# Optimization experiments

Hardware: AMD Instinct MI355X
Metric: run time of the kernel (lower is better)

The kernel has to match this reference:

```python
import jax, jax.numpy as jnp
import numpy as np

N = 8192      # nodes
E = 16384     # edges
G = 512       # graphs
IN = 235      # node feature dim (input_dim)
H = 64        # hidden_dim
ED = 52       # edge feature dim


def setup_inputs() -> dict:
    key = jax.random.key(0)
    ks = jax.random.split(key, 24)
    s = lambda fan_in: 1.0 / np.sqrt(fan_in)
    inp = {}
    inp["x"] = jax.random.normal(ks[0], (N, IN), dtype=jnp.float32)
    inp["edge_index"] = jax.random.randint(ks[1], (2, E), 0, N)
    inp["edge_attr"] = jax.random.uniform(ks[2], (E, ED), dtype=jnp.float32)
    inp["batch"] = jnp.sort(jax.random.randint(ks[3], (N,), 0, G))
    # EdgeModel (nn of nnconv1): Linear(52,128) -> Linear(128, 235*64)
    inp["W1"] = jax.random.normal(ks[4], (128, ED), dtype=jnp.float32) * s(ED)
    inp["b1"] = jnp.zeros((128,), jnp.float32)
    inp["W2"] = jax.random.normal(ks[5], (IN * H, 128), dtype=jnp.float32) * s(128)
    inp["b2"] = jnp.zeros((IN * H,), jnp.float32)
    # NNConv root weight and bias
    inp["root"] = jax.random.normal(ks[6], (IN, H), dtype=jnp.float32) * s(IN)
    inp["conv_b"] = jnp.zeros((H,), jnp.float32)
    # MLP head
    inp["fw1"] = jax.random.normal(ks[7], (128, H), dtype=jnp.float32) * s(H)
    inp["fb1"] = jnp.zeros((128,), jnp.float32)
    inp["fw2"] = jax.random.normal(ks[8], (256, 128), dtype=jnp.float32) * s(128)
    inp["fb2"] = jnp.zeros((256,), jnp.float32)
    inp["fw3"] = jax.random.normal(ks[9], (128, 256), dtype=jnp.float32) * s(256)
    inp["fb3"] = jnp.zeros((128,), jnp.float32)
    inp["fw4"] = jax.random.normal(ks[10], (1, 128), dtype=jnp.float32) * s(128)
    inp["fb4"] = jnp.zeros((1,), jnp.float32)
    return inp


def reference(x, edge_index, edge_attr, batch, W1, b1, W2, b2, root, conv_b,
              fw1, fb1, fw2, fb2, fw3, fb3, fw4, fb4):
    src, dst = edge_index[0], edge_index[1]
    # edge MLP -> per-edge weight matrices [E, IN, H]
    h = edge_attr @ W1.T + b1
    w = (h @ W2.T + b2).reshape(E, IN, H)
    # gather source node feats, per-edge matmul, scatter-add to destinations
    msg = jnp.einsum('ei,eih->eh', x[src], w)          # [E, H]
    agg = jax.ops.segment_sum(msg, dst, num_segments=N)  # [N, H]
    out = jax.nn.relu(agg + x @ root + conv_b)           # NNConv + ReLU
    # global mean pool per graph
    summ = jax.ops.segment_sum(out, batch, num_segments=G)
    cnt = jax.ops.segment_sum(jnp.ones((N, 1), out.dtype), batch, num_segments=G)
    pooled = summ / jnp.maximum(cnt, 1.0)                # [G, H]
    # dense MLP head
    y = jax.nn.relu(pooled @ fw1.T + fb1)
    y = jax.nn.relu(y @ fw2.T + fb2)
    y = jax.nn.relu(y @ fw3.T + fb3)
    return y @ fw4.T + fb4                               # [G, 1]
```

## Files before the change

kernel.cpp:

```cpp
#include <hip/hip_runtime.h>
#include <hip/hip_bf16.h>
#include <stdint.h>

#define N_NODES 8192
#define N_EDGES 16384
#define N_GRAPHS 512
#define IN_DIM 235
#define H_DIM 64
#define ED_DIM 52
#define HID1 128
#define KP 256
#define NB 3328
#define NBP 3584

#define BT_BLOCKS 940
#define EXT_BLOCKS 128
#define ZERO_BLOCKS 16
#define PREP_GRID (BT_BLOCKS + EXT_BLOCKS + ZERO_BLOCKS + N_NODES)

typedef __bf16 bf16x8 __attribute__((ext_vector_type(8)));
typedef float f32x4 __attribute__((ext_vector_type(4)));

static __device__ inline unsigned short f2bf(float f) {
    union { float f; unsigned u; } v; v.f = f;
    unsigned r = v.u + 0x7FFFu + ((v.u >> 16) & 1u);
    return (unsigned short)(r >> 16);
}

__global__ __launch_bounds__(256) void k_prep(const float* __restrict__ x,
                                              const float* __restrict__ W1,
                                              const float* __restrict__ W2,
                                              const float* __restrict__ b1,
                                              const float* __restrict__ b2,
                                              const float* __restrict__ root,
                                              unsigned short* __restrict__ A,
                                              unsigned short* __restrict__ Bt) {
    __shared__ float w1s[ED_DIM * 132];
    __shared__ float w2s[16 * 132];
    const int bx = blockIdx.x;
    const int t = threadIdx.x;

    if (bx < BT_BLOCKS) {
        const int i = bx >> 2;
        const int by = bx & 3;
        for (int j = t; j < ED_DIM * HID1; j += 256) {
            const int k = j / ED_DIM, d = j - k * ED_DIM;
            w1s[d * 132 + k] = W1[j];
        }
        const float* w2src = W2 + ((size_t)i * 64 + by * 16) * HID1;
        for (int j = t; j < 16 * HID1; j += 256) w2s[(j >> 7) * 132 + (j & 127)] = w2src[j];
        __syncthreads();
        const int hh = t & 15, dq = t >> 4;
        const float4* w2v = (const float4*)&w2s[hh * 132];
        #pragma unroll
        for (int m = 0; m < 4; ++m) {
            const int d = dq + m * 16;
            if (d >= ED_DIM) break;
            const float4* w1v = (const float4*)&w1s[d * 132];
            float acc = 0.f;
            #pragma unroll
            for (int k4 = 0; k4 < HID1 / 4; ++k4) {
                const float4 a = w1v[k4], b = w2v[k4];
                acc += a.x * b.x + a.y * b.y + a.z * b.z + a.w * b.w;
            }
            const int p = (by * 16 + hh) * ED_DIM + d;
            Bt[(size_t)p * KP + i] = f2bf(acc);
        }
    } else if (bx < BT_BLOCKS + EXT_BLOCKS) {
        const int j = bx - BT_BLOCKS;
        const int i = t;
        if (i < IN_DIM) {
            float v;
            if (j < 64) {
                v = root[i * H_DIM + j];
            } else {
                const int jj = i * H_DIM + (j - 64);
                float acc = b2[jj];
                const float* w = W2 + (size_t)jj * HID1;
                #pragma unroll 8
                for (int k = 0; k < HID1; ++k) acc += w[k] * b1[k];
                v = acc;
            }
            Bt[(size_t)(NB + j) * KP + i] = f2bf(v);
        }
    } else if (bx < BT_BLOCKS + EXT_BLOCKS + ZERO_BLOCKS) {
        const int z = bx - BT_BLOCKS - EXT_BLOCKS;
        const int R1 = NBP * 21;
        const int TOT = R1 + 128 * IN_DIM;
        for (int idx = z * 256 + t; idx < TOT; idx += ZERO_BLOCKS * 256) {
            size_t off;
            if (idx < R1) {
                const int r = idx / 21, c = IN_DIM + idx - (idx / 21) * 21;
                off = (size_t)r * KP + c;
            } else {
                const int k = idx - R1;
                const int r = 3456 + k / IN_DIM, c = k - (k / IN_DIM) * IN_DIM;
                off = (size_t)r * KP + c;
            }
            Bt[off] = 0;
        }
    } else {
        const int j = (bx - BT_BLOCKS - EXT_BLOCKS - ZERO_BLOCKS) * 256 + t;
        const int n = j >> 8, i = j & 255;
        A[j] = (i < IN_DIM) ? f2bf(x[n * IN_DIM + i]) : (unsigned short)0;
    }
}

__global__ __launch_bounds__(1024, 4) void k_gemm(const unsigned short* __restrict__ A,
                                                  const unsigned short* __restrict__ Bt,
                                                  unsigned short* __restrict__ P,
                                                  float* __restrict__ agg,
                                                  float* __restrict__ xb2,
                                                  const float* __restrict__ conv_b) {
    __shared__ unsigned short As[2 * 256 * 32];
    __shared__ unsigned short Bs[2 * 256 * 32];
    const int t = threadIdx.x;
    const int lin = blockIdx.x;
    const int xcd = lin & 7, bi = lin >> 3;
    const int mt = (bi / 14) * 8 + xcd;
    const int nt = bi % 14;
    const int m0 = mt * 256, n0 = nt * 256;
    const int wid = t >> 6, lane = t & 63;
    const int wm = wid & 3;
    const int wn = wid >> 2;
    const int q = lane >> 4, r16 = lane & 15;

    f32x4 acc[4][4] = {};

    auto stage = [&](int k0, int buf) {
        const int idx = t;
        const int row = idx >> 2;
        const int lgrp = ((idx & 3) ^ ((row >> 1) & 3)) * 8;
        const unsigned short* ga = &A[(size_t)(m0 + row) * KP + k0 + lgrp];
        const unsigned short* gb = &Bt[(size_t)(n0 + row) * KP + k0 + lgrp];
        char* la = (char*)As + buf * 16384 + wid * 1024;
        char* lb = (char*)Bs + buf * 16384 + wid * 1024;
        __builtin_amdgcn_global_load_lds(
            (const __attribute__((address_space(1))) unsigned int*)ga,
            (__attribute__((address_space(3))) unsigned int*)la, 16, 0, 0);
        __builtin_amdgcn_global_load_lds(
            (const __attribute__((address_space(1))) unsigned int*)gb,
            (__attribute__((address_space(3))) unsigned int*)lb, 16, 0, 0);
    };

    stage(0, 0);
    const int pcq = (q ^ ((r16 >> 1) & 3)) * 8;
    #pragma unroll
    for (int it = 0; it < 8; ++it) {
        __syncthreads();
        if (it < 7) stage((it + 1) * 32, (it + 1) & 1);
        const int bo = (it & 1) * 8192;
        bf16x8 af[4], bfr[4];
        #pragma unroll
        for (int mi = 0; mi < 4; ++mi)
            af[mi] = *(const bf16x8*)(&As[bo + (wm * 64 + mi * 16 + r16) * 32 + pcq]);
        #pragma unroll
        for (int ni = 0; ni < 4; ++ni)
            bfr[ni] = *(const bf16x8*)(&Bs[bo + (wn * 64 + ni * 16 + r16) * 32 + pcq]);
        #pragma unroll
        for (int mi = 0; mi < 4; ++mi)
            #pragma unroll
            for (int ni = 0; ni < 4; ++ni)
                acc[mi][ni] = __builtin_amdgcn_mfma_f32_16x16x32_bf16(
                    bfr[ni], af[mi], acc[mi][ni], 0, 0, 0);
    }

    if (n0 < NB) {
        #pragma unroll
        for (int mi = 0; mi < 4; ++mi)
            #pragma unroll
            for (int ni = 0; ni < 4; ++ni) {
                const int row = m0 + wm * 64 + mi * 16 + r16;
                const int col = n0 + wn * 64 + ni * 16 + q * 4;
                union { unsigned short us[4]; uint2 u2; } pk;
                #pragma unroll
                for (int rr = 0; rr < 4; ++rr) pk.us[rr] = f2bf(acc[mi][ni][rr]);
                *(uint2*)(&P[(size_t)row * NB + col]) = pk.u2;
            }
    } else if (wn < 2) {
        #pragma unroll
        for (int mi = 0; mi < 4; ++mi)
            #pragma unroll
            for (int ni = 0; ni < 4; ++ni) {
                const int row = m0 + wm * 64 + mi * 16 + r16;
                const int cl = ni * 16 + q * 4;
                if (wn == 0) {
                    const float4 cb = *(const float4*)&conv_b[cl];
                    float4 v;
                    v.x = acc[mi][ni][0] + cb.x; v.y = acc[mi][ni][1] + cb.y;
                    v.z = acc[mi][ni][2] + cb.z; v.w = acc[mi][ni][3] + cb.w;
                    *(float4*)(&agg[row * H_DIM + cl]) = v;
                } else {
                    float4 v;
                    v.x = acc[mi][ni][0]; v.y = acc[mi][ni][1];
                    v.z = acc[mi][ni][2]; v.w = acc[mi][ni][3];
                    *(float4*)(&xb2[row * H_DIM + cl]) = v;
                }
            }
    }
}

__global__ __launch_bounds__(256) void k_edge(const int* __restrict__ ei,
                                              const float* __restrict__ ea,
                                              const unsigned short* __restrict__ P,
                                              const float* __restrict__ xb2,
                                              float* __restrict__ agg) {
    const int e = (blockIdx.x * 256 + threadIdx.x) >> 6;
    const int h = threadIdx.x & 63;
    if (e >= N_EDGES) return;
    const int s = ei[e], dst = ei[N_EDGES + e];
    const uint2* Pr = (const uint2*)(P + (size_t)s * NB + h * ED_DIM);
    const float4* ev = (const float4*)(ea + (size_t)e * ED_DIM);

    uint2 pv[13];
    #pragma unroll
    for (int j = 0; j < 13; ++j) pv[j] = Pr[j];
    float4 eav[13];
    #pragma unroll
    for (int j = 0; j < 13; ++j) eav[j] = ev[j];

    float acc = xb2[s * H_DIM + h];
    #pragma unroll
    for (int j = 0; j < 13; ++j) {
        union { unsigned u; float f; } a0, a1, b0, b1;
        a0.u = pv[j].x << 16; a1.u = pv[j].x & 0xffff0000u;
        b0.u = pv[j].y << 16; b1.u = pv[j].y & 0xffff0000u;
        acc += eav[j].x * a0.f + eav[j].y * a1.f
             + eav[j].z * b0.f + eav[j].w * b1.f;
    }
    atomicAdd(&agg[dst * H_DIM + h], acc);
}

__global__ __launch_bounds__(256) void k_tail(const float* __restrict__ agg,
                                              const int* __restrict__ batch,
                                              const float* __restrict__ fw1, const float* __restrict__ fb1,
                                              const float* __restrict__ fw2, const float* __restrict__ fb2,
                                              const float* __restrict__ fw3, const float* __restrict__ fb3,
                                              const float* __restrict__ fw4, const float* __restrict__ fb4,
                                              float* __restrict__ out) {
    __shared__ float red[256];
    __shared__ float sp[64], s1[128], s2[256], s3[128];
    const int g = blockIdx.x, t = threadIdx.x;

    int lo = 0, hi = N_NODES;
    while (lo < hi) { const int mid = (lo + hi) >> 1; if (batch[mid] < g) lo = mid + 1; else hi = mid; }
    const int start = lo;
    hi = N_NODES;
    while (lo < hi) { const int mid = (lo + hi) >> 1; if (batch[mid] <= g) lo = mid + 1; else hi = mid; }
    const int end = lo;
    const float inv = 1.0f / fmaxf((float)(end - start), 1.0f);

    float a = 0.f;
    for (int n = start + (t >> 6); n < end; n += 4)
        a += fmaxf(agg[n * H_DIM + (t & 63)], 0.f);
    red[t] = a;
    __syncthreads();
    if (t < 64) sp[t] = (red[t] + red[t + 64] + red[t + 128] + red[t + 192]) * inv;
    __syncthreads();

    if (t < 128) {
        float acc = fb1[t];
        const float* w = fw1 + t * 64;
        #pragma unroll 8
        for (int k = 0; k < 64; ++k) acc += sp[k] * w[k];
        s1[t] = fmaxf(acc, 0.f);
    }
    __syncthreads();
    {
        float acc = fb2[t];
        const float* w = fw2 + t * 128;
        #pragma unroll 8
        for (int k = 0; k < 128; ++k) acc += s1[k] * w[k];
        s2[t] = fmaxf(acc, 0.f);
    }
    __syncthreads();
    if (t < 128) {
        float acc = fb3[t];
        const float* w = fw3 + t * 256;
        #pragma unroll 8
        for (int k = 0; k < 256; ++k) acc += s2[k] * w[k];
        s3[t] = fmaxf(acc, 0.f);
    }
    __syncthreads();
    if (t < 64) {
        float p = s3[t] * fw4[t] + s3[t + 64] * fw4[t + 64];
        #pragma unroll
        for (int off = 32; off > 0; off >>= 1) p += __shfl_down(p, off);
        if (t == 0) out[g] = p + fb4[0];
    }
}

extern "C" void kernel_launch(void* const* d_in, const int* in_sizes, int n_in,
                              void* d_out, int out_size, void* d_ws, size_t ws_size,
                              hipStream_t stream) {
    const float* x      = (const float*)d_in[0];
    const int*   ei     = (const int*)d_in[1];
    const float* ea     = (const float*)d_in[2];
    const int*   batch  = (const int*)d_in[3];
    const float* W1     = (const float*)d_in[4];
    const float* b1     = (const float*)d_in[5];
    const float* W2     = (const float*)d_in[6];
    const float* b2     = (const float*)d_in[7];
    const float* root   = (const float*)d_in[8];
    const float* conv_b = (const float*)d_in[9];
    const float* fw1 = (const float*)d_in[10]; const float* fb1 = (const float*)d_in[11];
    const float* fw2 = (const float*)d_in[12]; const float* fb2 = (const float*)d_in[13];
    const float* fw3 = (const float*)d_in[14]; const float* fb3 = (const float*)d_in[15];
    const float* fw4 = (const float*)d_in[16]; const float* fb4 = (const float*)d_in[17];
    float* out = (float*)d_out;

    char* ws = (char*)d_ws;
    unsigned short* A   = (unsigned short*)(ws);
    unsigned short* Bt  = (unsigned short*)(ws + 4194304);
    unsigned short* P   = (unsigned short*)(ws + 6029312);
    float* agg  = (float*)(ws + 60555264);
    float* xb2  = (float*)(ws + 62652416);

    k_prep<<<dim3(PREP_GRID), dim3(256), 0, stream>>>(x, W1, W2, b1, b2, root, A, Bt);
    k_gemm<<<dim3(448), dim3(1024), 0, stream>>>(A, Bt, P, agg, xb2, conv_b);
    k_edge<<<dim3(N_EDGES / 4), dim3(256), 0, stream>>>(ei, ea, P, xb2, agg);
    k_tail<<<dim3(N_GRAPHS), dim3(256), 0, stream>>>(agg, batch, fw1, fb1, fw2, fb2, fw3, fb3, fw4, fb4, out);
}
```

Before: 185.5 us.

## Shrink GEMM tiles to 128x128, interleave P layout, vectorize prep and tail

The GEMM tile drops from 256x256 with 1024 threads to 128x128 with 256 threads, over a 1728-block grid. This gives more, smaller blocks and removes the 1/4 idle-tail waste on the extension columns. The Bt/P column layout is permuted so that each edge thread reads P with a stride of 64 uint2, coalescing the per-edge gathers, and the zero-padding logic is simplified to match. The prep kernel converts x to bf16 eight elements per thread, and the bias-fold and tail MLP loops use float4 loads. Smaller tiles lower data reuse per block and raise global traffic for A and Bt.

```diff
diff --git a/kernel.cpp b/kernel.cpp
--- a/kernel.cpp
+++ b/kernel.cpp
@@ -13,10 +13,14 @@
 #define NB 3328
 #define NBP 3584
 
+
 #define BT_BLOCKS 940
 #define EXT_BLOCKS 128
 #define ZERO_BLOCKS 16
-#define PREP_GRID (BT_BLOCKS + EXT_BLOCKS + ZERO_BLOCKS + N_NODES)
+#define A_BLOCKS 1024
+#define PREP_GRID (BT_BLOCKS + EXT_BLOCKS + ZERO_BLOCKS + A_BLOCKS)
+
+#define GEMM_GRID 1728
 
 typedef __bf16 bf16x8 __attribute__((ext_vector_type(8)));
 typedef float f32x4 __attribute__((ext_vector_type(4)));
@@ -51,6 +55,7 @@
         for (int j = t; j < 16 * HID1; j += 256) w2s[(j >> 7) * 132 + (j & 127)] = w2src[j];
         __syncthreads();
         const int hh = t & 15, dq = t >> 4;
+        const int h = by * 16 + hh;
         const float4* w2v = (const float4*)&w2s[hh * 132];
         #pragma unroll
         for (int m = 0; m < 4; ++m) {
@@ -63,7 +68,7 @@
                 const float4 a = w1v[k4], b = w2v[k4];
                 acc += a.x * b.x + a.y * b.y + a.z * b.z + a.w * b.w;
             }
-            const int p = (by * 16 + hh) * ED_DIM + d;
+            const int p = ((d >> 2) << 8) + h * 4 + (d & 3);
             Bt[(size_t)p * KP + i] = f2bf(acc);
         }
     } else if (bx < BT_BLOCKS + EXT_BLOCKS) {
@@ -76,71 +81,76 @@
             } else {
                 const int jj = i * H_DIM + (j - 64);
                 float acc = b2[jj];
-                const float* w = W2 + (size_t)jj * HID1;
-                #pragma unroll 8
-                for (int k = 0; k < HID1; ++k) acc += w[k] * b1[k];
+                const float4* w = (const float4*)(W2 + (size_t)jj * HID1);
+                const float4* bv = (const float4*)b1;
+                #pragma unroll
+                for (int k4 = 0; k4 < HID1 / 4; ++k4) {
+                    const float4 a = w[k4], b = bv[k4];
+                    acc += a.x * b.x; acc += a.y * b.y; acc += a.z * b.z; acc += a.w * b.w;
+                }
                 v = acc;
             }
             Bt[(size_t)(NB + j) * KP + i] = f2bf(v);
         }
     } else if (bx < BT_BLOCKS + EXT_BLOCKS + ZERO_BLOCKS) {
         const int z = bx - BT_BLOCKS - EXT_BLOCKS;
-        const int R1 = NBP * 21;
-        const int TOT = R1 + 128 * IN_DIM;
+        const int TOT = 3456 * 21;
         for (int idx = z * 256 + t; idx < TOT; idx += ZERO_BLOCKS * 256) {
-            size_t off;
-            if (idx < R1) {
-                const int r = idx / 21, c = IN_DIM + idx - (idx / 21) * 21;
-                off = (size_t)r * KP + c;
-            } else {
-                const int k = idx - R1;
-                const int r = 3456 + k / IN_DIM, c = k - (k / IN_DIM) * IN_DIM;
-                off = (size_t)r * KP + c;
-            }
-            Bt[off] = 0;
+            const int r = idx / 21, c = IN_DIM + idx - r * 21;
+            Bt[(size_t)r * KP + c] = 0;
         }
     } else {
-        const int j = (bx - BT_BLOCKS - EXT_BLOCKS - ZERO_BLOCKS) * 256 + t;
-        const int n = j >> 8, i = j & 255;
-        A[j] = (i < IN_DIM) ? f2bf(x[n * IN_DIM + i]) : (unsigned short)0;
-    }
-}
-
-__global__ __launch_bounds__(1024, 4) void k_gemm(const unsigned short* __restrict__ A,
-                                                  const unsigned short* __restrict__ Bt,
-                                                  unsigned short* __restrict__ P,
-                                                  float* __restrict__ agg,
-                                                  float* __restrict__ xb2,
-                                                  const float* __restrict__ conv_b) {
-    __shared__ unsigned short As[2 * 256 * 32];
-    __shared__ unsigned short Bs[2 * 256 * 32];
+        const int j8 = (bx - BT_BLOCKS - EXT_BLOCKS - ZERO_BLOCKS) * 256 + t;
+        const int n = j8 >> 5, i0 = (j8 & 31) * 8;
+        const float* xr = x + (size_t)n * IN_DIM;
+        union { unsigned short us[8]; uint4 q; } pk;
+        #pragma unroll
+        for (int k = 0; k < 8; ++k) {
+            const int i = i0 + k;
+            pk.us[k] = (i < IN_DIM) ? f2bf(xr[i]) : (unsigned short)0;
+        }
+        *(uint4*)(&A[(size_t)j8 * 8]) = pk.q;
+    }
+}
+
+__global__ __launch_bounds__(256) void k_gemm(const unsigned short* __restrict__ A,
+                                              const unsigned short* __restrict__ Bt,
+                                              unsigned short* __restrict__ P,
+                                              float* __restrict__ agg,
+                                              float* __restrict__ xb2,
+                                              const float* __restrict__ conv_b) {
+    __shared__ unsigned short As[2 * 128 * 32];
+    __shared__ unsigned short Bs[2 * 128 * 32];
     const int t = threadIdx.x;
     const int lin = blockIdx.x;
     const int xcd = lin & 7, bi = lin >> 3;
-    const int mt = (bi / 14) * 8 + xcd;
-    const int nt = bi % 14;
-    const int m0 = mt * 256, n0 = nt * 256;
+    const int mt = (bi / 27) * 8 + xcd;
+    const int nt = bi % 27;
+    const int m0 = mt * 128, n0 = nt * 128;
     const int wid = t >> 6, lane = t & 63;
-    const int wm = wid & 3;
-    const int wn = wid >> 2;
+    const int wm = wid & 1;
+    const int wn = wid >> 1;
     const int q = lane >> 4, r16 = lane & 15;
 
     f32x4 acc[4][4] = {};
 
     auto stage = [&](int k0, int buf) {
-        const int idx = t;
-        const int row = idx >> 2;
-        const int lgrp = ((idx & 3) ^ ((row >> 1) & 3)) * 8;
-        const unsigned short* ga = &A[(size_t)(m0 + row) * KP + k0 + lgrp];
-        const unsigned short* gb = &Bt[(size_t)(n0 + row) * KP + k0 + lgrp];
-        char* la = (char*)As + buf * 16384 + wid * 1024;
-        char* lb = (char*)Bs + buf * 16384 + wid * 1024;
-        __builtin_amdgcn_global_load_lds(
-            (const __attribute__((address_space(1))) unsigned int*)ga,
-            (__attribute__((address_space(3))) unsigned int*)la, 16, 0, 0);
-        __builtin_amdgcn_global_load_lds(
-            (const __attribute__((address_space(1))) unsigned int*)gb,
-            (__attribute__((address_space(3))) unsigned int*)lb, 16, 0, 0);
+        #pragma unroll
+        for (int s = 0; s < 2; ++s) {
+            const int idx = s * 256 + t;
+            const int row = idx >> 2;
+            const int lgrp = ((idx & 3) ^ ((row >> 1) & 3)) * 8;
+            const unsigned short* ga = &A[(size_t)(m0 + row) * KP + k0 + lgrp];
+            const unsigned short* gb = &Bt[(size_t)(n0 + row) * KP + k0 + lgrp];
+            char* la = (char*)As + buf * 8192 + s * 4096 + wid * 1024;
+            char* lb = (char*)Bs + buf * 8192 + s * 4096 + wid * 1024;
+            __builtin_amdgcn_global_load_lds(
+                (const __attribute__((address_space(1))) unsigned int*)ga,
+                (__attribute__((address_space(3))) unsigned int*)la, 16, 0, 0);
+            __builtin_amdgcn_global_load_lds(
+                (const __attribute__((address_space(1))) unsigned int*)gb,
+                (__attribute__((address_space(3))) unsigned int*)lb, 16, 0, 0);
+        }
     };
 
     stage(0, 0);
@@ -149,7 +159,7 @@
     for (int it = 0; it < 8; ++it) {
         __syncthreads();
         if (it < 7) stage((it + 1) * 32, (it + 1) & 1);
-        const int bo = (it & 1) * 8192;
+        const int bo = (it & 1) * 4096;
         bf16x8 af[4], bfr[4];
         #pragma unroll
         for (int mi = 0; mi < 4; ++mi)
@@ -165,7 +175,7 @@
                     bfr[ni], af[mi], acc[mi][ni], 0, 0, 0);
     }
 
-    if (n0 < NB) {
+    if (nt < 26) {
         #pragma unroll
         for (int mi = 0; mi < 4; ++mi)
             #pragma unroll
@@ -177,7 +187,7 @@
                 for (int rr = 0; rr < 4; ++rr) pk.us[rr] = f2bf(acc[mi][ni][rr]);
                 *(uint2*)(&P[(size_t)row * NB + col]) = pk.u2;
             }
-    } else if (wn < 2) {
+    } else {
         #pragma unroll
         for (int mi = 0; mi < 4; ++mi)
             #pragma unroll
@@ -209,12 +219,12 @@
     const int h = threadIdx.x & 63;
     if (e >= N_EDGES) return;
     const int s = ei[e], dst = ei[N_EDGES + e];
-    const uint2* Pr = (const uint2*)(P + (size_t)s * NB + h * ED_DIM);
+    const uint2* Pr = (const uint2*)(P + (size_t)s * NB);
     const float4* ev = (const float4*)(ea + (size_t)e * ED_DIM);
 
     uint2 pv[13];
     #pragma unroll
-    for (int j = 0; j < 13; ++j) pv[j] = Pr[j];
+    for (int j = 0; j < 13; ++j) pv[j] = Pr[j * 64 + h];
     float4 eav[13];
     #pragma unroll
     for (int j = 0; j < 13; ++j) eav[j] = ev[j];
@@ -238,8 +248,11 @@
                                               const float* __restrict__ fw3, const float* __restrict__ fb3,
                                               const float* __restrict__ fw4, const float* __restrict__ fb4,
                                               float* __restrict__ out) {
-    __shared__ float red[256];
-    __shared__ float sp[64], s1[128], s2[256], s3[128];
+    __shared__ __align__(16) float red[256];
+    __shared__ __align__(16) float sp[64];
+    __shared__ __align__(16) float s1[128];
+    __shared__ __align__(16) float s2[256];
+    __shared__ __align__(16) float s3[128];
     const int g = blockIdx.x, t = threadIdx.x;
 
     int lo = 0, hi = N_NODES;
@@ -260,25 +273,37 @@
 
     if (t < 128) {
         float acc = fb1[t];
-        const float* w = fw1 + t * 64;
-        #pragma unroll 8
-        for (int k = 0; k < 64; ++k) acc += sp[k] * w[k];
+        const float4* w = (const float4*)(fw1 + t * 64);
+        const float4* sv = (const float4*)sp;
+        #pragma unroll
+        for (int k = 0; k < 16; ++k) {
+            const float4 a4 = w[k], b4 = sv[k];
+            acc += a4.x * b4.x; acc += a4.y * b4.y; acc += a4.z * b4.z; acc += a4.w * b4.w;
+        }
         s1[t] = fmaxf(acc, 0.f);
     }
     __syncthreads();
     {
         float acc = fb2[t];
-        const float* w = fw2 + t * 128;
-        #pragma unroll 8
-        for (int k = 0; k < 128; ++k) acc += s1[k] * w[k];
+        const float4* w = (const float4*)(fw2 + t * 128);
+        const float4* sv = (const float4*)s1;
+        #pragma unroll
+        for (int k = 0; k < 32; ++k) {
+            const float4 a4 = w[k], b4 = sv[k];
+            acc += a4.x * b4.x; acc += a4.y * b4.y; acc += a4.z * b4.z; acc += a4.w * b4.w;
+        }
         s2[t] = fmaxf(acc, 0.f);
     }
     __syncthreads();
     if (t < 128) {
         float acc = fb3[t];
-        const float* w = fw3 + t * 256;
-        #pragma unroll 8
-        for (int k = 0; k < 256; ++k) acc += s2[k] * w[k];
+        const float4* w = (const float4*)(fw3 + t * 256);
+        const float4* sv = (const float4*)s2;
+        #pragma unroll
+        for (int k = 0; k < 64; ++k) {
+            const float4 a4 = w[k], b4 = sv[k];
+            acc += a4.x * b4.x; acc += a4.y * b4.y; acc += a4.z * b4.z; acc += a4.w * b4.w;
+        }
         s3[t] = fmaxf(acc, 0.f);
     }
     __syncthreads();
@@ -317,7 +342,7 @@
     float* xb2  = (float*)(ws + 62652416);
 
     k_prep<<<dim3(PREP_GRID), dim3(256), 0, stream>>>(x, W1, W2, b1, b2, root, A, Bt);
-    k_gemm<<<dim3(448), dim3(1024), 0, stream>>>(A, Bt, P, agg, xb2, conv_b);
+    k_gemm<<<dim3(GEMM_GRID), dim3(256), 0, stream>>>(A, Bt, P, agg, xb2, conv_b);
     k_edge<<<dim3(N_EDGES / 4), dim3(256), 0, stream>>>(ei, ea, P, xb2, agg);
     k_tail<<<dim3(N_GRAPHS), dim3(256), 0, stream>>>(agg, batch, fw1, fb1, fw2, fb2, fw3, fb3, fw4, fb4, out);
 }
```

Result: no change. 185.9 us (+0.2%).
